# Performance work log

Measured on AMD Instinct MI355X. Metric: run time of the kernel, lower is better.

The kernel has to match this reference:

```python
import jax, jax.numpy as jnp
import numpy as np

N, E, D, STEPS, MOLS, OUT = 50000, 400000, 128, 3, 256, 32


def setup_inputs() -> dict:
    key = jax.random.key(0)
    ks = jax.random.split(key, 20)
    s = 0.1  # weight scale ~ 1/sqrt(fan_in) to keep relu chain stable
    inp = {
        "states": jax.random.normal(ks[0], (N, D), jnp.float32),
        "Win": jax.random.normal(ks[1], (STEPS, 2 * D, 64), jnp.float32) * s,
        "b_in": jax.random.normal(ks[2], (STEPS, 64), jnp.float32) * s,
        "Wh": jax.random.normal(ks[3], (STEPS, 64, 64), jnp.float32) * s,
        "b_h": jax.random.normal(ks[4], (STEPS, 64), jnp.float32) * s,
        "Wout": jax.random.normal(ks[5], (STEPS, 64, D), jnp.float32) * s,
        "b_out": jax.random.normal(ks[6], (STEPS, D), jnp.float32) * s,
        "fc1_w": jax.random.normal(ks[7], (D, 64), jnp.float32) * s,
        "fc1_b": jax.random.normal(ks[8], (64,), jnp.float32) * s,
        "fc2_w": jax.random.normal(ks[9], (64, 64), jnp.float32) * s,
        "fc2_b": jax.random.normal(ks[10], (64,), jnp.float32) * s,
        "out_w": jax.random.normal(ks[11], (64, OUT), jnp.float32) * s,
        "out_b": jax.random.normal(ks[12], (OUT,), jnp.float32) * s,
        "src": jax.random.randint(ks[13], (E,), 0, N, jnp.int32).astype(jnp.int64),
        "dst": jax.random.randint(ks[14], (E,), 0, N, jnp.int32).astype(jnp.int64),
        "mol_ids": jax.random.randint(ks[15], (N,), 0, MOLS, jnp.int32).astype(jnp.int64),
        "num_mols": MOLS,
    }
    return inp


def reference(states, Win, b_in, Wh, b_h, Wout, b_out,
              fc1_w, fc1_b, fc2_w, fc2_b, out_w, out_b,
              src, dst, mol_ids, num_mols):
    n_atoms = states.shape[0]
    s = states
    for t in range(Win.shape[0]):  # message_steps (small, static)
        # per-edge message input: concat(owner state, neighbor state) -> [E, 2D]
        x = jnp.concatenate([s[dst], s[src]], axis=-1)
        m = jax.nn.relu(x @ Win[t] + b_in[t])
        m = jax.nn.relu(m @ Wh[t] + b_h[t])
        m = jax.nn.relu(m @ Wout[t] + b_out[t])  # [E, D]
        # atom-wise sum aggregation of incoming messages
        s = jax.ops.segment_sum(m, dst, num_segments=n_atoms)
    # molecule representation: sum of final atom states per molecule
    mol_repr = jax.ops.segment_sum(s, mol_ids, num_segments=num_mols)  # [M, D]
    h = jax.nn.relu(mol_repr @ fc1_w + fc1_b)
    h = jax.nn.relu(h @ fc2_w + fc2_b)
    return h @ out_w + out_b  # [M, OUT]
```

## Files before the change

### kernel.cpp

```cpp
#include <hip/hip_runtime.h>

typedef unsigned long long u64;
typedef unsigned short ushort_t;

#define NA 50000
#define NE 400000
#define DF 128
#define HID 64
#define NMOL 256
#define NOUT 32
#define NSTEP 3
#define NPB 782

#define RNG 8192
#define NRNG 7
#define NCH 64
#define CHUNK 6250
#define NCHM 16
#define CHM 3125
#define NWB 336
#define HISTB (NRNG*NCH + NCHM + NWB)
#define SCATB (NRNG*NCH + NCHM)
#define MBUF_ROWS 160000

typedef __attribute__((ext_vector_type(8))) unsigned short ushort8;
typedef __attribute__((ext_vector_type(4))) float f32x4;
typedef __attribute__((ext_vector_type(8))) _Float16 half8;
typedef __attribute__((ext_vector_type(2))) _Float16 half2_t;
typedef __attribute__((ext_vector_type(2))) __fp16 fp16x2;

static __device__ __forceinline__ ushort_t f2h(float f) {
  union { _Float16 h; ushort_t u; } v; v.h = (_Float16)f; return v.u;
}
static __device__ __forceinline__ float hlo(unsigned d) {
  union { unsigned u; half2_t h; } v; v.u = d; return (float)v.h[0];
}
static __device__ __forceinline__ float hhi(unsigned d) {
  union { unsigned u; half2_t h; } v; v.u = d; return (float)v.h[1];
}
static __device__ __forceinline__ unsigned pkrtz(float a, float b) {
  union { fp16x2 h; unsigned u; } v;
  v.h = __builtin_amdgcn_cvt_pkrtz(a, b);
  return v.u;
}

__global__ __launch_bounds__(256) void hist_all(
    const int* __restrict__ dst, const int* __restrict__ mol_ids,
    const float* __restrict__ Win, const float* __restrict__ Wh,
    const float* __restrict__ Wout,
    ushort_t* __restrict__ WpB, ushort_t* __restrict__ WhB,
    ushort_t* __restrict__ WoB,
    ushort_t* __restrict__ H, unsigned* __restrict__ MH,
    int* __restrict__ mcnt) {
  __shared__ unsigned hist[RNG];
  const int b = blockIdx.x, t = threadIdx.x;
  if (b < NRNG * NCH) {
    const int r = b / NCH, c = b % NCH;
    const int lo = r * RNG;
    for (int i = t; i < RNG; i += 256) hist[i] = 0;
    __syncthreads();
    const int base = c * CHUNK;
    for (int k = t; k < CHUNK; k += 256) {
      int d = dst[base + k];
      unsigned rel = (unsigned)(d - lo);
      if (rel < RNG) atomicAdd(&hist[rel], 1u);
    }
    __syncthreads();
    ushort_t* Hp = H + (u64)b * RNG;
    for (int i = t; i < RNG; i += 256) Hp[i] = (ushort_t)hist[i];
    return;
  }
  int b2 = b - NRNG * NCH;
  if (b2 < NCHM) {
    if (t < 256) hist[t] = 0;
    __syncthreads();
    const int base = b2 * CHM;
    for (int k = t; k < CHM; k += 256) atomicAdd(&hist[mol_ids[base + k]], 1u);
    __syncthreads();
    if (t < 256) {
      MH[b2 * 256 + t] = hist[t];
      if (hist[t]) atomicAdd(&mcnt[t], (int)hist[t]);
    }
    return;
  }
  int g = (b2 - NCHM) * 256 + t;
  if (g < 3 * 16384) {
    int tt = g / 16384, r = g % 16384;
    int j = r & 7, lane = (r >> 3) & 63, f = r >> 9;
    int kc = f & 3, nt = f >> 2;
    int k = kc * 32 + (lane >> 4) * 8 + j;
    int n = nt * 16 + (lane & 15);
    float v = (n < 64) ? Win[tt * 16384 + k * 64 + n]
                       : Win[tt * 16384 + (128 + k) * 64 + (n - 64)];
    WpB[g] = f2h(v);
  }
  int g2 = g - 3 * 16384;
  if (g2 >= 0 && g2 < 3 * 4096) {
    int tt = g2 / 4096, r = g2 % 4096;
    int j = r & 7, lane = (r >> 3) & 63, f = r >> 9;
    int kc = f & 1, nt = f >> 1;
    int k = kc * 32 + (lane >> 4) * 8 + j;
    int n = nt * 16 + (lane & 15);
    WhB[g2] = f2h(Wh[tt * 4096 + k * 64 + n]);
  }
  int g3 = g2 - 3 * 4096;
  if (g3 >= 0 && g3 < 3 * 8192) {
    int tt = g3 / 8192, r = g3 % 8192;
    int j = r & 7, lane = (r >> 3) & 63, f = r >> 9;
    int kc = f & 1, nt = f >> 1;
    int k = kc * 32 + (lane >> 4) * 8 + j;
    int n = nt * 16 + (lane & 15);
    WoB[g3] = f2h(Wout[tt * 8192 + k * 128 + n]);
  }
}

__global__ void col_scan(const ushort_t* __restrict__ H,
                         ushort_t* __restrict__ Orel, int* __restrict__ counts) {
  int bidx = blockIdx.x * 256 + threadIdx.x;
  if (bidx >= NA) return;
  int r = bidx >> 13, i = bidx & (RNG - 1);
  const ushort_t* Hp = H + ((u64)r * NCH) * RNG + i;
  unsigned acc = 0;
  for (int c = 0; c < NCH; c++) {
    Orel[(u64)c * NA + bidx] = (ushort_t)acc;
    acc += Hp[(u64)c * RNG];
  }
  counts[bidx] = (int)acc;
}

__global__ void scan_phase1(const int* __restrict__ counts, int* __restrict__ tmp,
                            int* __restrict__ blk,
                            const int* __restrict__ mcnt, int* __restrict__ mrow) {
  __shared__ int sh[1024];
  int t = threadIdx.x;
  int i = blockIdx.x * 1024 + t;
  sh[t] = (i < NA) ? counts[i] : 0;
  __syncthreads();
  for (int off = 1; off < 1024; off <<= 1) {
    int x = (t >= off) ? sh[t - off] : 0;
    __syncthreads();
    sh[t] += x;
    __syncthreads();
  }
  if (i < NA) tmp[i] = sh[t];
  if (t == 1023) blk[blockIdx.x] = sh[1023];
  if (blockIdx.x == gridDim.x - 1) {
    __syncthreads();
    sh[t] = (t < NMOL) ? mcnt[t] : 0;
    __syncthreads();
    for (int off = 1; off < NMOL; off <<= 1) {
      int x = (t >= off && t < NMOL) ? sh[t - off] : 0;
      __syncthreads();
      if (t < NMOL) sh[t] += x;
      __syncthreads();
    }
    if (t < NMOL) mrow[t + 1] = sh[t];
    if (t == 0) mrow[0] = 0;
  }
}

__global__ void scan_phase3(const int* __restrict__ tmp, const int* __restrict__ blk,
                            int* __restrict__ row_ptr,
                            int* __restrict__ ntmp, int* __restrict__ nblk) {
  __shared__ int sh[1024];
  __shared__ int spre_sh;
  int t = threadIdx.x;
  int bid = blockIdx.x;
  if (t < 64) {
    int v = (t < bid) ? blk[t] : 0;
    for (int off = 32; off; off >>= 1) v += __shfl_down(v, off);
    if (t == 0) spre_sh = v;
  }
  __syncthreads();
  int spre = spre_sh;
  int i = bid * 1024 + t;
  int nwin = 0;
  if (i < NA) {
    int re = tmp[i] + spre;
    int rs = (t == 0) ? spre : (tmp[i - 1] + spre);
    row_ptr[i + 1] = re;
    if (re > rs) nwin = ((re - 1) >> 2) - (rs >> 2) + 1;
  }
  if (i == 0) row_ptr[0] = 0;
  sh[t] = nwin;
  __syncthreads();
  for (int off = 1; off < 1024; off <<= 1) {
    int x = (t >= off) ? sh[t - off] : 0;
    __syncthreads();
    sh[t] += x;
    __syncthreads();
  }
  if (i < NA) ntmp[i] = sh[t];
  if (t == 1023) nblk[bid] = sh[1023];
}

__global__ void nscan_p3(const int* __restrict__ ntmp, const int* __restrict__ nblk,
                         const int* __restrict__ row_ptr,
                         int* __restrict__ orow, int* __restrict__ orow2) {
  __shared__ int spre_sh;
  int t = threadIdx.x;
  int bid = blockIdx.x;
  if (t < 64) {
    int v = (t < bid) ? nblk[t] : 0;
    for (int off = 32; off; off >>= 1) v += __shfl_down(v, off);
    if (t == 0) spre_sh = v;
  }
  __syncthreads();
  int spre = spre_sh;
  int i = bid * 1024 + t;
  if (i < NA) {
    orow[i + 1] = ntmp[i] + spre;
    int oi = (t == 0) ? spre : (ntmp[i - 1] + spre);
    orow2[i] = oi - (row_ptr[i] >> 2);
  }
  if (i == 0) orow[0] = 0;
}

__global__ __launch_bounds__(256) void scat_all(
    const int* __restrict__ dst, const int* __restrict__ src,
    const int* __restrict__ row_ptr, const ushort_t* __restrict__ Orel,
    unsigned* __restrict__ ds_pack,
    const int* __restrict__ mol_ids, const int* __restrict__ mrow,
    const unsigned* __restrict__ MH, int* __restrict__ mol_sorted) {
  __shared__ unsigned cnt[RNG];
  __shared__ unsigned mbase[256];
  const int b = blockIdx.x, t = threadIdx.x;
  if (b < NRNG * NCH) {
    const int r = b / NCH, c = b % NCH;
    const int lo = r * RNG;
    for (int i = t; i < RNG; i += 256) cnt[i] = 0;
    __syncthreads();
    const int base = c * CHUNK;
    const ushort_t* Op = Orel + (u64)c * NA;
    for (int k = t; k < CHUNK; k += 256) {
      int e = base + k;
      int d = dst[e];
      unsigned rel = (unsigned)(d - lo);
      if (rel < RNG) {
        unsigned lr = atomicAdd(&cnt[rel], 1u);
        int pos = row_ptr[d] + (int)Op[d] + (int)lr;
        ds_pack[pos] = ((unsigned)d << 16) | (unsigned)src[e];
      }
    }
    return;
  }
  const int c2 = b - NRNG * NCH;
  if (t < 256) {
    unsigned s = (unsigned)mrow[t];
    for (int cp = 0; cp < c2; cp++) s += MH[cp * 256 + t];
    mbase[t] = s;
    cnt[t] = 0;
  }
  __syncthreads();
  const int base = c2 * CHM;
  for (int k = t; k < CHM; k += 256) {
    int a = base + k;
    int m = mol_ids[a];
    unsigned lr = atomicAdd(&cnt[m], 1u);
    mol_sorted[mbase[m] + lr] = a;
  }
}

__global__ __launch_bounds__(256) void node_proj(
    const float* __restrict__ s_in, const ushort_t* __restrict__ WpB,
    const float* __restrict__ b_in, ushort_t* __restrict__ PQb) {
  const int t = threadIdx.x;
  const int lane = t & 63, wv = t >> 6, quad = lane >> 4, l15 = lane & 15;
  const int n0 = blockIdx.x * 64 + wv * 16;
  int n = n0 + l15; if (n >= NA) n = NA - 1;
  union { half8 v; unsigned d[4]; } a[4];
#pragma unroll
  for (int c = 0; c < 4; c++) {
    const float* p = s_in + (u64)n * 128 + c * 32 + quad * 8;
    float4 f0 = *(const float4*)(p);
    float4 f1 = *(const float4*)(p + 4);
    a[c].d[0] = pkrtz(f0.x, f0.y);
    a[c].d[1] = pkrtz(f0.z, f0.w);
    a[c].d[2] = pkrtz(f1.x, f1.y);
    a[c].d[3] = pkrtz(f1.z, f1.w);
  }
  float binv[4];
#pragma unroll
  for (int nt = 0; nt < 4; nt++) binv[nt] = b_in[nt * 16 + l15];
#pragma unroll
  for (int nt = 0; nt < 8; nt++) {
    f32x4 acc = {0.f, 0.f, 0.f, 0.f};
#pragma unroll
    for (int c = 0; c < 4; c++) {
      half8 b = *(const half8*)&WpB[((nt * 4 + c) * 64 + lane) * 8];
      acc = __builtin_amdgcn_mfma_f32_16x16x32_f16(a[c].v, b, acc, 0, 0, 0);
    }
    float bias = (nt < 4) ? binv[nt] : 0.f;
#pragma unroll
    for (int r = 0; r < 4; r++) {
      int nn = n0 + quad * 4 + r;
      if (nn < NA) PQb[(u64)nn * 128 + nt * 16 + l15] = f2h(acc[r] + bias);
    }
  }
}

__global__ __launch_bounds__(256) void edge_msg(
    const ushort_t* __restrict__ PQb,
    const ushort_t* __restrict__ WhB, const ushort_t* __restrict__ WoB,
    const float* __restrict__ b_h, const float* __restrict__ b_out,
    const unsigned* __restrict__ ds_pack, const int* __restrict__ orow2,
    unsigned* __restrict__ m_buf) {
  __shared__ unsigned eps[64];
  __shared__ int ops[64];
  __shared__ ushort_t h2s[4][16 * 72];
  const int t = threadIdx.x;
  const int lane = t & 63, wv = t >> 6, quad = lane >> 4, l15 = lane & 15;
  const long long e0 = (long long)blockIdx.x * 64;

  if (t < 64) {
    long long e = e0 + t;
    unsigned pk = ds_pack[e];
    eps[t] = pk;
    ops[t] = orow2[pk >> 16] + (int)(e >> 2);
  }
  float bh[4], bo[8];
#pragma unroll
  for (int nt = 0; nt < 4; nt++) bh[nt] = b_h[nt * 16 + l15];
#pragma unroll
  for (int nt = 0; nt < 8; nt++) bo[nt] = b_out[nt * 16 + l15];
  __syncthreads();

  union PQ { ushort8 v; half2_t h[4]; } pv[2], qv[2];
  {
    unsigned pk = eps[wv * 16 + l15];
    int da = pk >> 16, sa = pk & 0xffffu;
#pragma unroll
    for (int c = 0; c < 2; c++) {
      const int col = c * 32 + quad * 8;
      pv[c].v = *(const ushort8*)&PQb[(u64)da * 128 + col];
      qv[c].v = *(const ushort8*)&PQb[(u64)sa * 128 + 64 + col];
    }
  }

  const half2_t z2 = {(_Float16)0.f, (_Float16)0.f};
  const int ebl = wv * 16;

  union { half8 v; half2_t h[4]; } a1[2];
#pragma unroll
  for (int c = 0; c < 2; c++) {
#pragma unroll
    for (int k = 0; k < 4; k++) {
      half2_t s = pv[c].h[k] + qv[c].h[k];
      a1[c].h[k] = __builtin_elementwise_max(s, z2);
    }
  }

  ushort_t* hb = h2s[wv];
#pragma unroll
  for (int nt = 0; nt < 4; nt++) {
    f32x4 acc = {0.f, 0.f, 0.f, 0.f};
#pragma unroll
    for (int c = 0; c < 2; c++) {
      half8 b = *(const half8*)&WhB[((nt * 2 + c) * 64 + lane) * 8];
      acc = __builtin_amdgcn_mfma_f32_16x16x32_f16(a1[c].v, b, acc, 0, 0, 0);
    }
#pragma unroll
    for (int r = 0; r < 4; r++)
      hb[(quad * 4 + r) * 72 + nt * 16 + l15] =
          f2h(fmaxf(acc[r] + bh[nt], 0.f));
  }

  half8 a2[2];
#pragma unroll
  for (int c = 0; c < 2; c++)
    a2[c] = *(const half8*)&hb[l15 * 72 + c * 32 + quad * 8];

  f32x4 acc2[8];
#pragma unroll
  for (int nt = 0; nt < 8; nt++) {
    f32x4 acc = {0.f, 0.f, 0.f, 0.f};
#pragma unroll
    for (int c = 0; c < 2; c++) {
      half8 b = *(const half8*)&WoB[((nt * 2 + c) * 64 + lane) * 8];
      acc = __builtin_amdgcn_mfma_f32_16x16x32_f16(a2[c], b, acc, 0, 0, 0);
    }
    acc2[nt] = acc;
  }

  {
    const int base = ebl + quad * 4;
    int prev = (int)(eps[base] >> 16);
    int orow_ = ops[base];
    float run[8];
#pragma unroll
    for (int nt = 0; nt < 8; nt++) run[nt] = 0.f;
#pragma unroll
    for (int r = 0; r < 4; r++) {
      int er = base + r;
      int dcur = (int)(eps[er] >> 16);
      if (dcur != prev) {
        unsigned* rowp = m_buf + (u64)orow_ * 64;
#pragma unroll
        for (int k = 0; k < 4; k++)
          rowp[k * 16 + l15] = pkrtz(run[2 * k], run[2 * k + 1]);
#pragma unroll
        for (int nt = 0; nt < 8; nt++) run[nt] = 0.f;
        prev = dcur; orow_ = ops[er];
      }
#pragma unroll
      for (int nt = 0; nt < 8; nt++)
        run[nt] += fmaxf(acc2[nt][r] + bo[nt], 0.f);
    }
    unsigned* rowp = m_buf + (u64)orow_ * 64;
#pragma unroll
    for (int k = 0; k < 4; k++)
      rowp[k * 16 + l15] = pkrtz(run[2 * k], run[2 * k + 1]);
  }
}

__global__ __launch_bounds__(256) void agg_proj(
    const unsigned* __restrict__ m_buf, const int* __restrict__ orow,
    const ushort_t* __restrict__ WpB, const float* __restrict__ b_in,
    ushort_t* __restrict__ PQb) {
  __shared__ ushort_t a_s[64 * 136];
  __shared__ int obs_s[65];
  const int t = threadIdx.x;
  const int lane = t & 63, wv = t >> 6, quad = lane >> 4, l15 = lane & 15;
  const int n0 = blockIdx.x * 64;
  if (t < 65) {
    int idx = n0 + t; if (idx > NA) idx = NA;
    obs_s[t] = orow[idx];
  }
  __syncthreads();

  for (int r = 0; r < 16; r++) {
    const int d = n0 + wv * 16 + r;
    float s0 = 0.f, s1 = 0.f;
    if (d < NA) {
      int ob = obs_s[wv * 16 + r], oe = obs_s[wv * 16 + r + 1];
      int n = oe - ob;
      float t0 = 0.f, t1 = 0.f, u0 = 0.f, u1 = 0.f, v0 = 0.f, v1 = 0.f;
      int full = n & ~3;
      int e = ob;
      for (; e < ob + full; e += 4) {
        unsigned w0 = m_buf[(u64)(e + 0) * 64 + lane];
        unsigned w1 = m_buf[(u64)(e + 1) * 64 + lane];
        unsigned w2 = m_buf[(u64)(e + 2) * 64 + lane];
        unsigned w3 = m_buf[(u64)(e + 3) * 64 + lane];
        s0 += hlo(w0); s1 += hhi(w0);
        t0 += hlo(w1); t1 += hhi(w1);
        u0 += hlo(w2); u1 += hhi(w2);
        v0 += hlo(w3); v1 += hhi(w3);
      }
      int rem = n - full;
      if (rem > 0) {
        int i1 = (rem > 1) ? e + 1 : e;
        int i2 = (rem > 2) ? e + 2 : e;
        unsigned w0 = m_buf[(u64)e * 64 + lane];
        unsigned w1 = m_buf[(u64)i1 * 64 + lane];
        unsigned w2 = m_buf[(u64)i2 * 64 + lane];
        s0 += hlo(w0); s1 += hhi(w0);
        if (rem > 1) { t0 += hlo(w1); t1 += hhi(w1); }
        if (rem > 2) { u0 += hlo(w2); u1 += hhi(w2); }
      }
      s0 = (s0 + t0) + (u0 + v0);
      s1 = (s1 + t1) + (u1 + v1);
    }
    const int row = wv * 16 + r;
    a_s[row * 136 + quad * 32 + l15] = f2h(s0);
    a_s[row * 136 + quad * 32 + 16 + l15] = f2h(s1);
  }

  float binv[4];
#pragma unroll
  for (int nt = 0; nt < 4; nt++) binv[nt] = b_in[nt * 16 + l15];
  half8 a[4];
#pragma unroll
  for (int c = 0; c < 4; c++)
    a[c] = *(const half8*)&a_s[(wv * 16 + l15) * 136 + c * 32 + quad * 8];
#pragma unroll
  for (int nt = 0; nt < 8; nt++) {
    f32x4 acc = {0.f, 0.f, 0.f, 0.f};
#pragma unroll
    for (int c = 0; c < 4; c++) {
      half8 b = *(const half8*)&WpB[((nt * 4 + c) * 64 + lane) * 8];
      acc = __builtin_amdgcn_mfma_f32_16x16x32_f16(a[c], b, acc, 0, 0, 0);
    }
    float bias = (nt < 4) ? binv[nt] : 0.f;
#pragma unroll
    for (int r = 0; r < 4; r++) {
      int nn = n0 + wv * 16 + quad * 4 + r;
      if (nn < NA) PQb[(u64)nn * 128 + nt * 16 + l15] = f2h(acc[r] + bias);
    }
  }
}

__global__ __launch_bounds__(256) void agg_mol2(
    const unsigned* __restrict__ m_buf, const int* __restrict__ orow,
    const int* __restrict__ mol_sorted, const int* __restrict__ mol_ids,
    float* __restrict__ mol_repr) {
  __shared__ int mids[64], obs[64], oes[64];
  const int t = threadIdx.x;
  const int lane = t & 63, wv = t >> 6;
  const int base = blockIdx.x * 64;
  if (t < 64) {
    int idx = base + t;
    int r = (idx < NA) ? mol_sorted[idx] : 0;
    mids[t] = (idx < NA) ? mol_ids[r] : -1;
    obs[t] = orow[r];
    oes[t] = orow[r + 1];
  }
  __syncthreads();
  const int c0 = (lane >> 4) * 32 + (lane & 15);
  float r0 = 0.f, r1 = 0.f;
  int prev = mids[wv * 16];
  for (int i = 0; i < 16; i++) {
    int li = wv * 16 + i;
    int m = mids[li];
    if (m != prev) {
      if (prev >= 0) {
        atomicAdd(&mol_repr[(u64)prev * 128 + c0], r0);
        atomicAdd(&mol_repr[(u64)prev * 128 + c0 + 16], r1);
      }
      r0 = 0.f; r1 = 0.f; prev = m;
    }
    if (m >= 0) {
      int ob = obs[li], oe = oes[li];
      int n = oe - ob;
      float t0 = 0.f, t1 = 0.f, u0 = 0.f, u1 = 0.f, v0 = 0.f, v1 = 0.f;
      int full = n & ~3;
      int e = ob;
      for (; e < ob + full; e += 4) {
        unsigned w0 = m_buf[(u64)(e + 0) * 64 + lane];
        unsigned w1 = m_buf[(u64)(e + 1) * 64 + lane];
        unsigned w2 = m_buf[(u64)(e + 2) * 64 + lane];
        unsigned w3 = m_buf[(u64)(e + 3) * 64 + lane];
        r0 += hlo(w0); r1 += hhi(w0);
        t0 += hlo(w1); t1 += hhi(w1);
        u0 += hlo(w2); u1 += hhi(w2);
        v0 += hlo(w3); v1 += hhi(w3);
      }
      int rem = n - full;
      if (rem > 0) {
        int i1 = (rem > 1) ? e + 1 : e;
        int i2 = (rem > 2) ? e + 2 : e;
        unsigned w0 = m_buf[(u64)e * 64 + lane];
        unsigned w1 = m_buf[(u64)i1 * 64 + lane];
        unsigned w2 = m_buf[(u64)i2 * 64 + lane];
        r0 += hlo(w0); r1 += hhi(w0);
        if (rem > 1) { t0 += hlo(w1); t1 += hhi(w1); }
        if (rem > 2) { u0 += hlo(w2); u1 += hhi(w2); }
      }
      r0 += (t0 + u0) + v0;
      r1 += (t1 + u1) + v1;
    }
  }
  if (prev >= 0) {
    atomicAdd(&mol_repr[(u64)prev * 128 + c0], r0);
    atomicAdd(&mol_repr[(u64)prev * 128 + c0 + 16], r1);
  }
}

__global__ void final_mlp(const float* __restrict__ mol_repr,
                          const float* __restrict__ fc1_w, const float* __restrict__ fc1_b,
                          const float* __restrict__ fc2_w, const float* __restrict__ fc2_b,
                          const float* __restrict__ out_w, const float* __restrict__ out_b,
                          float* __restrict__ out) {
  int m = blockIdx.x, j = threadIdx.x;
  __shared__ float h1sh[64], h2sh[64];
  const float* mr = mol_repr + (u64)m * DF;
  float acc = fc1_b[j];
  for (int d = 0; d < DF; d++) acc = fmaf(mr[d], fc1_w[d * 64 + j], acc);
  h1sh[j] = fmaxf(acc, 0.f);
  __syncthreads();
  acc = fc2_b[j];
  for (int k = 0; k < 64; k++) acc = fmaf(h1sh[k], fc2_w[k * 64 + j], acc);
  h2sh[j] = fmaxf(acc, 0.f);
  __syncthreads();
  if (j < NOUT) {
    acc = out_b[j];
    for (int k = 0; k < 64; k++) acc = fmaf(h2sh[k], out_w[k * NOUT + j], acc);
    out[(u64)m * NOUT + j] = acc;
  }
}

extern "C" void kernel_launch(void* const* d_in, const int* in_sizes, int n_in,
                              void* d_out, int out_size, void* d_ws, size_t ws_size,
                              hipStream_t stream) {
  const float* states = (const float*)d_in[0];
  const float* Win    = (const float*)d_in[1];
  const float* b_in   = (const float*)d_in[2];
  const float* Wh     = (const float*)d_in[3];
  const float* b_h    = (const float*)d_in[4];
  const float* Wout   = (const float*)d_in[5];
  const float* b_out  = (const float*)d_in[6];
  const float* fc1_w  = (const float*)d_in[7];
  const float* fc1_b  = (const float*)d_in[8];
  const float* fc2_w  = (const float*)d_in[9];
  const float* fc2_b  = (const float*)d_in[10];
  const float* out_w  = (const float*)d_in[11];
  const float* out_b  = (const float*)d_in[12];
  const int* src      = (const int*)d_in[13];
  const int* dst      = (const int*)d_in[14];
  const int* mol_ids  = (const int*)d_in[15];

  char* ws = (char*)d_ws;
  u64 o = 0;
  auto alloc = [&](u64 bytes) {
    void* p = ws + o;
    o += (bytes + 255) & ~255ull;
    return p;
  };
  unsigned* m_buf = (unsigned*)alloc((u64)MBUF_ROWS * 64 * 4);
  ushort_t* PQb  = (ushort_t*)alloc((u64)NA * DF * 2);
  ushort_t* WpB  = (ushort_t*)alloc(3 * 16384 * 2);
  ushort_t* WhB  = (ushort_t*)alloc(3 * 4096 * 2);
  ushort_t* WoB  = (ushort_t*)alloc(3 * 8192 * 2);
  char* zbase    = ws + o;
  float* molr    = (float*)alloc((u64)NMOL * DF * 4);
  int* mcnt      = (int*)alloc(NMOL * 4);
  u64 zbytes     = (u64)((ws + o) - zbase);
  int* counts    = (int*)alloc((u64)NA * 4);
  int* row_ptr   = (int*)alloc((u64)(NA + 1) * 4);
  int* mrow      = (int*)alloc((NMOL + 1) * 4);
  unsigned* ds_pack = (unsigned*)alloc((u64)NE * 4);
  int* mol_sorted = (int*)alloc((u64)NA * 4);
  int* scan_tmp  = (int*)alloc((u64)NA * 4);
  int* blk_sums  = (int*)alloc(64 * 4);
  int* ntmp      = (int*)alloc((u64)NA * 4);
  int* nblk      = (int*)alloc(64 * 4);
  int* orow      = (int*)alloc((u64)(NA + 1) * 4);
  int* orow2     = (int*)alloc((u64)NA * 4);
  ushort_t* H    = (ushort_t*)alloc((u64)NRNG * NCH * RNG * 2);
  ushort_t* Orel = (ushort_t*)alloc((u64)NCH * NA * 2);
  unsigned* MH   = (unsigned*)alloc((u64)NCHM * 256 * 4);
  (void)ws_size; (void)in_sizes; (void)n_in; (void)out_size;

  const int NSCAN = (NA + 1023) / 1024;

  hipMemsetAsync(zbase, 0, zbytes, stream);

  hist_all<<<HISTB, 256, 0, stream>>>(dst, mol_ids, Win, Wh, Wout,
                                      WpB, WhB, WoB, H, MH, mcnt);
  col_scan<<<(NA + 255) / 256, 256, 0, stream>>>(H, Orel, counts);
  scan_phase1<<<NSCAN, 1024, 0, stream>>>(counts, scan_tmp, blk_sums, mcnt, mrow);
  scan_phase3<<<NSCAN, 1024, 0, stream>>>(scan_tmp, blk_sums, row_ptr, ntmp, nblk);
  nscan_p3<<<NSCAN, 1024, 0, stream>>>(ntmp, nblk, row_ptr, orow, orow2);
  scat_all<<<SCATB, 256, 0, stream>>>(dst, src, row_ptr, Orel, ds_pack,
                                      mol_ids, mrow, MH, mol_sorted);

  node_proj<<<NPB, 256, 0, stream>>>(states, WpB, b_in, PQb);
  for (int t = 0; t < NSTEP; t++) {
    edge_msg<<<NE / 64, 256, 0, stream>>>(
        PQb, WhB + t * 4096, WoB + t * 8192,
        b_h + t * 64, b_out + t * 128, ds_pack, orow2, m_buf);
    if (t < NSTEP - 1) {
      agg_proj<<<(NA + 63) / 64, 256, 0, stream>>>(m_buf, orow,
                                                   WpB + (t + 1) * 16384,
                                                   b_in + (t + 1) * 64, PQb);
    } else {
      agg_mol2<<<(NA + 63) / 64, 256, 0, stream>>>(m_buf, orow, mol_sorted,
                                                   mol_ids, molr);
    }
  }
  final_mlp<<<NMOL, 64, 0, stream>>>(molr, fc1_w, fc1_b, fc2_w, fc2_b, out_w, out_b,
                                     (float*)d_out);
}
```

Measured before the change: 304.7 us.

## Make edge_msg persistent with software-pipelined gathers across edge tiles

The edge message kernel becomes a persistent grid of 1024 blocks, with each wave looping over 16-edge tiles. Index loads are issued two tiles ahead and feature gathers one tile ahead, so gather latency overlaps with the MFMA work of the current tile. Shared-memory staging of edge packs and the block barrier are replaced by cross-lane shuffles. The cost is higher register pressure from carrying three contexts and fewer resident blocks to hide latency by occupancy.

```diff
diff --git a/kernel.cpp b/kernel.cpp
--- a/kernel.cpp
+++ b/kernel.cpp
@@ -22,6 +22,10 @@
 #define HISTB (NRNG*NCH + NCHM + NWB)
 #define SCATB (NRNG*NCH + NCHM)
 #define MBUF_ROWS 160000
+
+#define NT (NE / 16)
+#define EBLK 1024
+#define EGW (EBLK * 4)
 
 typedef __attribute__((ext_vector_type(8))) unsigned short ushort8;
 typedef __attribute__((ext_vector_type(4))) float f32x4;
@@ -305,94 +309,94 @@
     const float* __restrict__ b_h, const float* __restrict__ b_out,
     const unsigned* __restrict__ ds_pack, const int* __restrict__ orow2,
     unsigned* __restrict__ m_buf) {
-  __shared__ unsigned eps[64];
-  __shared__ int ops[64];
   __shared__ ushort_t h2s[4][16 * 72];
   const int t = threadIdx.x;
   const int lane = t & 63, wv = t >> 6, quad = lane >> 4, l15 = lane & 15;
-  const long long e0 = (long long)blockIdx.x * 64;
-
-  if (t < 64) {
-    long long e = e0 + t;
-    unsigned pk = ds_pack[e];
-    eps[t] = pk;
-    ops[t] = orow2[pk >> 16] + (int)(e >> 2);
-  }
+  const int gw = blockIdx.x * 4 + wv;
+
   float bh[4], bo[8];
 #pragma unroll
   for (int nt = 0; nt < 4; nt++) bh[nt] = b_h[nt * 16 + l15];
 #pragma unroll
   for (int nt = 0; nt < 8; nt++) bo[nt] = b_out[nt * 16 + l15];
-  __syncthreads();
-
-  union PQ { ushort8 v; half2_t h[4]; } pv[2], qv[2];
-  {
-    unsigned pk = eps[wv * 16 + l15];
-    int da = pk >> 16, sa = pk & 0xffffu;
-#pragma unroll
-    for (int c = 0; c < 2; c++) {
-      const int col = c * 32 + quad * 8;
-      pv[c].v = *(const ushort8*)&PQb[(u64)da * 128 + col];
-      qv[c].v = *(const ushort8*)&PQb[(u64)sa * 128 + 64 + col];
-    }
-  }
-
+
+  ushort_t* hb = h2s[wv];
+  const int colq = quad * 8;
   const half2_t z2 = {(_Float16)0.f, (_Float16)0.f};
-  const int ebl = wv * 16;
-
-  union { half8 v; half2_t h[4]; } a1[2];
-#pragma unroll
-  for (int c = 0; c < 2; c++) {
+
+  struct Ctx {
+    int e;
+    unsigned pk;
+    int o;
+    ushort8 pv0, pv1, qv0, qv1;
+  };
+
+  auto load_pk = [&](Ctx& c, int tile) {
+    c.e = tile * 16 + l15;
+    c.pk = ds_pack[c.e];
+  };
+  auto gather = [&](Ctx& c) {
+    u64 da = c.pk >> 16, sa = c.pk & 0xffffu;
+    c.o = orow2[da] + (c.e >> 2);
+    c.pv0 = *(const ushort8*)&PQb[da * 128 + colq];
+    c.pv1 = *(const ushort8*)&PQb[da * 128 + 32 + colq];
+    c.qv0 = *(const ushort8*)&PQb[sa * 128 + 64 + colq];
+    c.qv1 = *(const ushort8*)&PQb[sa * 128 + 96 + colq];
+  };
+  auto compute = [&](Ctx& c) {
+    union UPQ { ushort8 u; half2_t h[4]; };
+    UPQ P0, P1, Q0, Q1;
+    P0.u = c.pv0; P1.u = c.pv1; Q0.u = c.qv0; Q1.u = c.qv1;
+    union { half8 v; half2_t h[4]; } a1[2];
 #pragma unroll
     for (int k = 0; k < 4; k++) {
-      half2_t s = pv[c].h[k] + qv[c].h[k];
-      a1[c].h[k] = __builtin_elementwise_max(s, z2);
-    }
-  }
-
-  ushort_t* hb = h2s[wv];
-#pragma unroll
-  for (int nt = 0; nt < 4; nt++) {
-    f32x4 acc = {0.f, 0.f, 0.f, 0.f};
-#pragma unroll
-    for (int c = 0; c < 2; c++) {
-      half8 b = *(const half8*)&WhB[((nt * 2 + c) * 64 + lane) * 8];
-      acc = __builtin_amdgcn_mfma_f32_16x16x32_f16(a1[c].v, b, acc, 0, 0, 0);
-    }
-#pragma unroll
-    for (int r = 0; r < 4; r++)
-      hb[(quad * 4 + r) * 72 + nt * 16 + l15] =
-          f2h(fmaxf(acc[r] + bh[nt], 0.f));
-  }
-
-  half8 a2[2];
-#pragma unroll
-  for (int c = 0; c < 2; c++)
-    a2[c] = *(const half8*)&hb[l15 * 72 + c * 32 + quad * 8];
-
-  f32x4 acc2[8];
-#pragma unroll
-  for (int nt = 0; nt < 8; nt++) {
-    f32x4 acc = {0.f, 0.f, 0.f, 0.f};
-#pragma unroll
-    for (int c = 0; c < 2; c++) {
-      half8 b = *(const half8*)&WoB[((nt * 2 + c) * 64 + lane) * 8];
-      acc = __builtin_amdgcn_mfma_f32_16x16x32_f16(a2[c], b, acc, 0, 0, 0);
-    }
-    acc2[nt] = acc;
-  }
-
-  {
-    const int base = ebl + quad * 4;
-    int prev = (int)(eps[base] >> 16);
-    int orow_ = ops[base];
+      half2_t s0 = P0.h[k] + Q0.h[k];
+      half2_t s1 = P1.h[k] + Q1.h[k];
+      a1[0].h[k] = __builtin_elementwise_max(s0, z2);
+      a1[1].h[k] = __builtin_elementwise_max(s1, z2);
+    }
+#pragma unroll
+    for (int nt = 0; nt < 4; nt++) {
+      f32x4 acc = {0.f, 0.f, 0.f, 0.f};
+#pragma unroll
+      for (int cc = 0; cc < 2; cc++) {
+        half8 b = *(const half8*)&WhB[((nt * 2 + cc) * 64 + lane) * 8];
+        acc = __builtin_amdgcn_mfma_f32_16x16x32_f16(a1[cc].v, b, acc, 0, 0, 0);
+      }
+#pragma unroll
+      for (int r = 0; r < 4; r++)
+        hb[(quad * 4 + r) * 72 + nt * 16 + l15] =
+            f2h(fmaxf(acc[r] + bh[nt], 0.f));
+    }
+    half8 a2[2];
+    a2[0] = *(const half8*)&hb[l15 * 72 + colq];
+    a2[1] = *(const half8*)&hb[l15 * 72 + 32 + colq];
+    f32x4 acc2[8];
+#pragma unroll
+    for (int nt = 0; nt < 8; nt++) {
+      f32x4 acc = {0.f, 0.f, 0.f, 0.f};
+#pragma unroll
+      for (int cc = 0; cc < 2; cc++) {
+        half8 b = *(const half8*)&WoB[((nt * 2 + cc) * 64 + lane) * 8];
+        acc = __builtin_amdgcn_mfma_f32_16x16x32_f16(a2[cc], b, acc, 0, 0, 0);
+      }
+      acc2[nt] = acc;
+    }
+    int pkr[4], orr[4];
+#pragma unroll
+    for (int r = 0; r < 4; r++) {
+      int srcl = (lane & 48) + quad * 4 + r;
+      pkr[r] = __shfl((int)c.pk, srcl);
+      orr[r] = __shfl(c.o, srcl);
+    }
+    unsigned prev = ((unsigned)pkr[0]) >> 16;
+    int orow_ = orr[0];
     float run[8];
 #pragma unroll
     for (int nt = 0; nt < 8; nt++) run[nt] = 0.f;
 #pragma unroll
     for (int r = 0; r < 4; r++) {
-      int er = base + r;
-      int dcur = (int)(eps[er] >> 16);
+      unsigned dcur = ((unsigned)pkr[r]) >> 16;
       if (dcur != prev) {
         unsigned* rowp = m_buf + (u64)orow_ * 64;
 #pragma unroll
@@ -400,7 +404,7 @@
           rowp[k * 16 + l15] = pkrtz(run[2 * k], run[2 * k + 1]);
 #pragma unroll
         for (int nt = 0; nt < 8; nt++) run[nt] = 0.f;
-        prev = dcur; orow_ = ops[er];
+        prev = dcur; orow_ = orr[r];
       }
 #pragma unroll
       for (int nt = 0; nt < 8; nt++)
@@ -410,6 +414,22 @@
 #pragma unroll
     for (int k = 0; k < 4; k++)
       rowp[k * 16 + l15] = pkrtz(run[2 * k], run[2 * k + 1]);
+  };
+
+  Ctx A, B, C;
+  int tc = gw;
+  load_pk(A, tc);
+  int tb = tc + EGW;
+  if (tb < NT) load_pk(B, tb);
+  gather(A);
+  while (tc < NT) {
+    int tn = tc + EGW;
+    if (tn < NT) gather(B);
+    int t2 = tn + EGW;
+    if (t2 < NT) load_pk(C, t2);
+    compute(A);
+    A = B; B = C;
+    tc = tn;
   }
 }
 
@@ -646,7 +666,7 @@
 
   node_proj<<<NPB, 256, 0, stream>>>(states, WpB, b_in, PQb);
   for (int t = 0; t < NSTEP; t++) {
-    edge_msg<<<NE / 64, 256, 0, stream>>>(
+    edge_msg<<<EBLK, 256, 0, stream>>>(
         PQb, WhB + t * 4096, WoB + t * 8192,
         b_h + t * 64, b_out + t * 128, ds_pack, orow2, m_buf);
     if (t < NSTEP - 1) {
```

Result: faster. 284.0 us (-6.8%).
